# Performance work log

Hardware: AMD Instinct MI355X
Metric: run time of the kernel (lower is better)

The kernel has to match this reference:

```python
import jax, jax.numpy as jnp
import numpy as np

SCALE_DTYPE = jnp.float32

def rotate_half(x):
    half = x.shape[-1] // 2
    return jnp.concatenate([-x[..., half:], x[..., :half]], axis=-1)

def apply_rope(x, cos, sin):
    # x: [B,T,H,Dh]; cos/sin: [T,Dh] -> broadcast to [1,T,1,Dh]
    c = cos[None, :, None, :]
    s = sin[None, :, None, :]
    return x * c + rotate_half(x) * s

def setup_inputs() -> dict:
    key = jax.random.key(0)
    ks = jax.random.split(key, 7)
    B, T, D, H, Dh = 4, 2048, 1024, 16, 64
    x = jax.random.normal(ks[0], (B, T, D), dtype=jnp.float32)
    cos = jax.random.uniform(ks[1], (T, Dh), dtype=jnp.float32)
    sin = jax.random.uniform(ks[2], (T, Dh), dtype=jnp.float32)
    scale = 1.0 / np.sqrt(D)
    Wq = jax.random.normal(ks[3], (D, D), dtype=jnp.float32) * scale
    Wk = jax.random.normal(ks[4], (D, D), dtype=jnp.float32) * scale
    Wv = jax.random.normal(ks[5], (D, D), dtype=jnp.float32) * scale
    Wo = jax.random.normal(ks[6], (D, D), dtype=jnp.float32) * scale
    return {"x": x, "cos": cos, "sin": sin, "Wq": Wq, "Wk": Wk, "Wv": Wv, "Wo": Wo}

def reference(x, cos, sin, Wq, Wk, Wv, Wo):
    B, T, D = x.shape
    H, Dh = 16, 64
    # Linear projections (weights stored [in, out]) and split heads
    q = (x @ Wq).reshape(B, T, H, Dh)
    k = (x @ Wk).reshape(B, T, H, Dh)
    v = (x @ Wv).reshape(B, T, H, Dh)
    q = apply_rope(q, cos[:T], sin[:T])
    k = apply_rope(k, cos[:T], sin[:T])
    scale = 1.0 / jnp.sqrt(jnp.asarray(Dh, dtype=x.dtype))
    # [B,H,T,T] causal scores
    scores = jnp.einsum('bthd,bshd->bhts', q, k) * scale
    causal = jnp.tril(jnp.ones((T, T), dtype=bool))
    scores = jnp.where(causal[None, None, :, :], scores, jnp.asarray(-jnp.inf, dtype=scores.dtype))
    weights = jax.nn.softmax(scores, axis=-1)
    out = jnp.einsum('bhts,bshd->bthd', weights, v).reshape(B, T, D)
    return out @ Wo
```

## Files before the change

### kernel.cpp

```cpp
#include <hip/hip_runtime.h>
#include <cstdint>
#include <cstddef>

typedef unsigned short ushort_t;
typedef __attribute__((ext_vector_type(8))) short short8;
typedef __attribute__((ext_vector_type(4))) float float4v;
typedef __attribute__((ext_vector_type(4))) unsigned short ushort4v;

__device__ __forceinline__ float b2f(ushort_t u) {
    uint32_t x = ((uint32_t)u) << 16;
    float f;
    __builtin_memcpy(&f, &x, 4);
    return f;
}
__device__ __forceinline__ ushort_t f2b(float f) {
    uint32_t x;
    __builtin_memcpy(&x, &f, 4);
    uint32_t r = (x + 0x7fffu + ((x >> 16) & 1u)) >> 16;
    return (ushort_t)r;
}
__device__ __forceinline__ ushort_t f2b_trunc(float f) {
    uint32_t x;
    __builtin_memcpy(&x, &f, 4);
    return (ushort_t)(x >> 16);
}

typedef __attribute__((address_space(3))) void lds_void;
typedef __attribute__((address_space(1))) const void gbl_void;
__device__ __forceinline__ void gload16(const void* g, void* l) {
    __builtin_amdgcn_global_load_lds((gbl_void*)(uintptr_t)g, (lds_void*)(uintptr_t)l, 16, 0, 0);
}

__global__ void detect_dtype(const ushort_t* __restrict__ cosp, int* __restrict__ flag) {
    int tid = threadIdx.x;
    int bad = 0;
    for (int i = tid; i < 512; i += 64) {
        ushort_t u = cosp[i];
        int sign = u >> 15;
        int e = (u >> 7) & 0xFF;
        if (sign || e > 126) bad = 1;
    }
    int anybad = __any(bad);
    if (tid == 0) *flag = anybad ? 1 : 0;
}

__global__ __launch_bounds__(256) void convert_x(const void* __restrict__ in,
                                                 ushort_t* __restrict__ out,
                                                 const int* __restrict__ flag) {
    if (*flag == 0) return;
    int i = (blockIdx.x * 256 + threadIdx.x) * 4;
    float4v v = *(const float4v*)((const float*)in + i);
    ushort4v o;
#pragma unroll
    for (int j = 0; j < 4; ++j) o[j] = f2b(v[j]);
    *(ushort4v*)(out + i) = o;
}

__global__ __launch_bounds__(256) void convert_cs(const void* __restrict__ c,
                                                  const void* __restrict__ s,
                                                  ushort_t* __restrict__ cb,
                                                  ushort_t* __restrict__ sb,
                                                  const int* __restrict__ flag) {
    int f = *flag;
    int i = blockIdx.x * 256 + threadIdx.x;
    if (i >= 131072) return;
    if (f) {
        cb[i] = f2b(((const float*)c)[i]);
        sb[i] = f2b(((const float*)s)[i]);
    } else {
        cb[i] = ((const ushort_t*)c)[i];
        sb[i] = ((const ushort_t*)s)[i];
    }
}

__global__ __launch_bounds__(256) void transpose_w4(const void* __restrict__ w0,
                                                    const void* __restrict__ w1,
                                                    const void* __restrict__ w2,
                                                    const void* __restrict__ w3,
                                                    ushort_t* __restrict__ out,
                                                    const int* __restrict__ flag) {
    int f = *flag;
    int z = blockIdx.z;
    const void* in = (z == 0) ? w0 : (z == 1) ? w1 : (z == 2) ? w2 : w3;
    ushort_t* o = out + (size_t)z * 1024 * 1024;
    __shared__ ushort_t tile[32][33];
    int bx = blockIdx.x * 32;
    int by = blockIdx.y * 32;
    int tx = threadIdx.x & 31;
    int ty = threadIdx.x >> 5;
    for (int r = ty; r < 32; r += 8) {
        size_t idx = (size_t)(by + r) * 1024 + bx + tx;
        tile[r][tx] = f ? f2b(((const float*)in)[idx]) : ((const ushort_t*)in)[idx];
    }
    __syncthreads();
    for (int r = ty; r < 32; r += 8)
        o[(size_t)(bx + r) * 1024 + by + tx] = tile[tx][r];
}

template <int W>
__device__ __forceinline__ void vm_wait() {
    if constexpr (W == 6)      asm volatile("s_waitcnt vmcnt(6)" ::: "memory");
    else                       asm volatile("s_waitcnt vmcnt(0)" ::: "memory");
}
#define KBAR()                                       \
    do {                                             \
        asm volatile("" ::: "memory");               \
        __builtin_amdgcn_s_barrier();                \
        asm volatile("" ::: "memory");               \
    } while (0)

__global__ __launch_bounds__(512, 2) void gemm_qkv(const ushort_t* __restrict__ X0,
                                                   const ushort_t* __restrict__ X1,
                                                   const ushort_t* __restrict__ Wt,
                                                   ushort_t* __restrict__ qk,
                                                   ushort_t* __restrict__ vt,
                                                   const ushort_t* __restrict__ cosb,
                                                   const ushort_t* __restrict__ sinb,
                                                   const int* __restrict__ flagp) {
    __shared__ ushort_t LDS[73728];
    char* LDSc = (char*)LDS;

    int tid = threadIdx.x;
    int lane = tid & 63;
    int wave = tid >> 6;
    int wm = wave >> 1;
    int wn = wave & 1;
    int quad = lane >> 4;
    int l16 = lane & 15;

    int id = blockIdx.x;
    int xcd = id & 7;
    int r = id >> 3;
    int m0 = (xcd * 4 + (r & 3)) * 256;
    int n0 = (r >> 2) * 128;

    const ushort_t* Xb = (*flagp) ? X1 : X0;

    int lrow = lane >> 3;
    int lslot = (lane & 7) ^ lrow;
    const ushort_t* aSrc = Xb + (size_t)(m0 + wave * 32 + lrow) * 1024 + lslot * 8;
    const ushort_t* bSrc = Wt + (size_t)(n0 + wave * 16 + lrow) * 1024 + lslot * 8;
    int ldsA_w = (wave * 32) * 128;
    int ldsB_w = (wave * 16) * 128;

    int aoff0 = (wm * 64 + l16) * 128 + ((quad ^ (l16 & 7)) * 16);
    int aoff1 = (wm * 64 + l16) * 128 + (((4 + quad) ^ (l16 & 7)) * 16);
    int boff0 = (wn * 64 + l16) * 128 + ((quad ^ (l16 & 7)) * 16);
    int boff1 = (wn * 64 + l16) * 128 + (((4 + quad) ^ (l16 & 7)) * 16);

    float4v acc[4][4];
#pragma unroll
    for (int i = 0; i < 4; ++i)
#pragma unroll
        for (int n = 0; n < 4; ++n) acc[i][n] = (float4v){0.f, 0.f, 0.f, 0.f};

#define STAGE6(t, jj)                                                       \
    do {                                                                    \
        const ushort_t* as_ = aSrc + (jj) * 64;                             \
        const ushort_t* bs_ = bSrc + (jj) * 64;                             \
        char* al_ = LDSc + (t) * 32768 + ldsA_w;                            \
        char* bl_ = LDSc + 98304 + (t) * 16384 + ldsB_w;                    \
        gload16(as_, al_);                                                  \
        gload16(as_ + 8 * 1024, al_ + 1024);                                \
        gload16(as_ + 16 * 1024, al_ + 2048);                               \
        gload16(as_ + 24 * 1024, al_ + 3072);                               \
        gload16(bs_, bl_);                                                  \
        gload16(bs_ + 8 * 1024, bl_ + 1024);                                \
    } while (0)

#define COMPUTE(t)                                                          \
    do {                                                                    \
        const char* ab_ = LDSc + (t) * 32768;                               \
        const char* bb_ = LDSc + 98304 + (t) * 16384;                       \
        short8 a0_[4], b0_[4], a1_[4], b1_[4];                              \
        _Pragma("unroll") for (int i = 0; i < 4; ++i) {                     \
            a0_[i] = *(const short8*)(ab_ + aoff0 + i * 2048);              \
            a1_[i] = *(const short8*)(ab_ + aoff1 + i * 2048);              \
        }                                                                   \
        _Pragma("unroll") for (int n = 0; n < 4; ++n) {                     \
            b0_[n] = *(const short8*)(bb_ + boff0 + n * 2048);              \
            b1_[n] = *(const short8*)(bb_ + boff1 + n * 2048);              \
        }                                                                   \
        __builtin_amdgcn_s_setprio(1);                                      \
        _Pragma("unroll") for (int i = 0; i < 4; ++i)                       \
            _Pragma("unroll") for (int n = 0; n < 4; ++n)                   \
                acc[i][n] = __builtin_amdgcn_mfma_f32_16x16x32_bf16(        \
                    a0_[i], b0_[n], acc[i][n], 0, 0, 0);                    \
        _Pragma("unroll") for (int i = 0; i < 4; ++i)                       \
            _Pragma("unroll") for (int n = 0; n < 4; ++n)                   \
                acc[i][n] = __builtin_amdgcn_mfma_f32_16x16x32_bf16(        \
                    a1_[i], b1_[n], acc[i][n], 0, 0, 0);                    \
        __builtin_amdgcn_s_setprio(0);                                      \
    } while (0)

    STAGE6(0, 0);
    STAGE6(1, 1);
    vm_wait<6>();
    KBAR();

#pragma unroll 1
    for (int g = 0; g < 4; ++g) {
        int j = g * 3;
        STAGE6(2, j + 2);
        COMPUTE(0);
        vm_wait<6>();
        KBAR();
        STAGE6(0, j + 3);
        COMPUTE(1);
        vm_wait<6>();
        KBAR();
        STAGE6(1, j + 4);
        COMPUTE(2);
        vm_wait<6>();
        KBAR();
    }
    STAGE6(2, 14);
    COMPUTE(0);
    vm_wait<6>();
    KBAR();
    STAGE6(0, 15);
    COMPUTE(1);
    vm_wait<6>();
    KBAR();
    COMPUTE(2);
    vm_wait<0>();
    KBAR();
    COMPUTE(0);

#undef STAGE6
#undef COMPUTE

    int nglob = n0 + wn * 64;
    int region = nglob >> 10;
    int hcol = (nglob & 1023) >> 6;

    if (region < 2) {
        float scl = (region == 0) ? 0.18033688f : 1.0f;
        int colbase = region * 1024 + hcol * 64 + l16;
#pragma unroll
        for (int i = 0; i < 4; ++i) {
            int rowb = m0 + wm * 64 + i * 16 + quad * 4;
#pragma unroll
            for (int rr = 0; rr < 4; ++rr) {
                int row = rowb + rr;
                int t = row & 2047;
                const ushort_t* cp = cosb + t * 64 + l16;
                const ushort_t* sp = sinb + t * 64 + l16;
                float c0 = b2f(cp[0]), c1 = b2f(cp[16]), c2 = b2f(cp[32]), c3 = b2f(cp[48]);
                float s0v = b2f(sp[0]), s1v = b2f(sp[16]), s2v = b2f(sp[32]), s3v = b2f(sp[48]);
                float a0 = acc[i][0][rr], a1 = acc[i][1][rr], a2 = acc[i][2][rr], a3 = acc[i][3][rr];
                float o0 = (a0 * c0 - a2 * s0v) * scl;
                float o1 = (a1 * c1 - a3 * s1v) * scl;
                float o2 = (a2 * c2 + a0 * s2v) * scl;
                float o3 = (a3 * c3 + a1 * s3v) * scl;
                size_t base = (size_t)row * 2048 + colbase;
                qk[base] = f2b(o0);
                qk[base + 16] = f2b(o1);
                qk[base + 32] = f2b(o2);
                qk[base + 48] = f2b(o3);
            }
        }
    } else {
#pragma unroll
        for (int i = 0; i < 4; ++i) {
            int rowb = m0 + wm * 64 + i * 16 + quad * 4;
            int b = rowb >> 11;
            int t0 = rowb & 2047;
            size_t hb = (size_t)(b * 16 + hcol) * 64;
#pragma unroll
            for (int n = 0; n < 4; ++n) {
                int d = l16 + n * 16;
                ushort4v pk;
#pragma unroll
                for (int rr = 0; rr < 4; ++rr) pk[rr] = f2b(acc[i][n][rr]);
                *(ushort4v*)(vt + (hb + d) * 2048 + t0) = pk;
            }
        }
    }
}

__global__ __launch_bounds__(256) void gemm_proj(const ushort_t* __restrict__ A, int lda,
                                                 const ushort_t* __restrict__ Bt,
                                                 void* __restrict__ C, int ldc,
                                                 int K,
                                                 const int* __restrict__ flagp) {
    __shared__ ushort_t Al[128 * 64];
    __shared__ ushort_t Bl[128 * 64];

    int tid = threadIdx.x;
    int lane = tid & 63;
    int wave = tid >> 6;
    int wr = wave >> 1;
    int wc = wave & 1;
    int quad = lane >> 4;
    int l16 = lane & 15;

    int id = blockIdx.x;
    int xcd = id & 7;
    int t = id >> 3;
    int m0 = (xcd * 8 + (t & 7)) * 128;
    int n0 = (t >> 3) * 128;

    int lrow = lane >> 3;
    int lcol = (lane & 7) * 8;

    float4v acc[4][4];
#pragma unroll
    for (int i = 0; i < 4; ++i)
#pragma unroll
        for (int j = 0; j < 4; ++j) acc[i][j] = (float4v){0.f, 0.f, 0.f, 0.f};

    for (int k0 = 0; k0 < K; k0 += 64) {
        __syncthreads();
#pragma unroll
        for (int p = 0; p < 4; ++p) {
            int row = wave * 32 + p * 8 + lrow;
            gload16(A + (size_t)(m0 + row) * lda + k0 + lcol, &Al[(size_t)(wave * 4 + p) * 512]);
            gload16(Bt + (size_t)(n0 + row) * K + k0 + lcol, &Bl[(size_t)(wave * 4 + p) * 512]);
        }
        __syncthreads();

#pragma unroll
        for (int ks = 0; ks < 2; ++ks) {
            int kf = ks * 32 + quad * 8;
            short8 a_frag[4], b_frag[4];
#pragma unroll
            for (int i = 0; i < 4; ++i) {
                a_frag[i] = *(const short8*)(&Al[(wr * 64 + i * 16 + l16) * 64 + kf]);
                b_frag[i] = *(const short8*)(&Bl[(wc * 64 + i * 16 + l16) * 64 + kf]);
            }
#pragma unroll
            for (int i = 0; i < 4; ++i)
#pragma unroll
                for (int j = 0; j < 4; ++j)
                    acc[i][j] = __builtin_amdgcn_mfma_f32_16x16x32_bf16(
                        a_frag[i], b_frag[j], acc[i][j], 0, 0, 0);
        }
    }

    int f32out = *flagp;

#pragma unroll
    for (int i = 0; i < 4; ++i) {
        int rowb = m0 + wr * 64 + i * 16 + quad * 4;
#pragma unroll
        for (int r = 0; r < 4; ++r) {
            size_t base = (size_t)(rowb + r) * ldc + n0 + wc * 64 + l16;
            if (f32out) {
                float* Cf = (float*)C;
#pragma unroll
                for (int j = 0; j < 4; ++j) Cf[base + j * 16] = acc[i][j][r];
            } else {
                ushort_t* Cb = (ushort_t*)C;
#pragma unroll
                for (int j = 0; j < 4; ++j) Cb[base + j * 16] = f2b(acc[i][j][r]);
            }
        }
    }
}

__global__ __launch_bounds__(512, 4) void attn_mfma(ushort_t* qk,
                                                    const ushort_t* __restrict__ vt) {
    __shared__ ushort_t Kl[2][4096];
    __shared__ ushort_t Vl[2][4096];
    __shared__ ushort_t Pl[8 * 16 * 72];

    int tid = threadIdx.x;
    int lane = tid & 63;
    int wave = tid >> 6;
    int quad = lane >> 4;
    int l16 = lane & 15;

    int id = blockIdx.x;
    int bxi = (id >> 3) & 7;
    int bh = (id & 7) * 8 + (id >> 6);
    int b = bh >> 4;
    int h = bh & 15;

    ushort_t* Pw = &Pl[wave * 16 * 72];

    int rr = tid >> 3;
    int sl = (tid & 7) ^ (rr & 7);
    const ushort_t* ksrc = qk + (size_t)(b * 2048 + rr) * 2048 + 1024 + h * 64 + sl * 8;
    const ushort_t* vsrc = vt + (size_t)(bh * 64 + rr) * 2048 + sl * 8;
    char* kdst = (char*)&Kl[0][0] + wave * 1024;
    char* vdst = (char*)&Vl[0][0] + wave * 1024;

    int swr = l16 & 7;

#pragma unroll 1
    for (int phase = 0; phase < 2; ++phase) {
        int qt = phase ? bxi : (15 - bxi);
        int row0 = qt * 128 + wave * 16;
        size_t qbase = ((size_t)(b * 2048 + row0)) * 2048 + h * 64;

        short8 qf[2];
        {
            const ushort_t* p = qk + qbase + (size_t)l16 * 2048 + quad * 8;
            qf[0] = *(const short8*)p;
            qf[1] = *(const short8*)(p + 32);
        }

        float4v oacc[4];
#pragma unroll
        for (int nt = 0; nt < 4; ++nt) oacc[nt] = (float4v){0.f, 0.f, 0.f, 0.f};
        float psum[4];
#pragma unroll
        for (int r = 0; r < 4; ++r) psum[r] = 0.f;

        int ntiles = 2 * qt + 2;

        gload16(ksrc, kdst);
        gload16(vsrc, vdst);
        vm_wait<0>();
        KBAR();

        for (int st = 0; st < ntiles; ++st) {
            int s0 = st * 64;
            int buf = st & 1;

            if (st + 1 < ntiles) {
                gload16(ksrc + (size_t)(s0 + 64) * 2048, kdst + ((st + 1) & 1) * 8192);
                gload16(vsrc + (s0 + 64), vdst + ((st + 1) & 1) * 8192);
            }

            if (s0 <= row0 + 15) {
                const char* kb = (const char*)&Kl[buf][0];
                const char* vb = (const char*)&Vl[buf][0];

                float4v sacc[4];
#pragma unroll
                for (int ct = 0; ct < 4; ++ct) sacc[ct] = (float4v){0.f, 0.f, 0.f, 0.f};
#pragma unroll
                for (int ks = 0; ks < 2; ++ks) {
                    short8 bfr[4];
#pragma unroll
                    for (int ct = 0; ct < 4; ++ct)
                        bfr[ct] = *(const short8*)(kb + (ct * 16 + l16) * 128 +
                                                   (((ks * 4 + quad) ^ swr) * 16));
                    __builtin_amdgcn_s_setprio(1);
#pragma unroll
                    for (int ct = 0; ct < 4; ++ct)
                        sacc[ct] = __builtin_amdgcn_mfma_f32_16x16x32_bf16(
                            qf[ks], bfr[ct], sacc[ct], 0, 0, 0);
                    __builtin_amdgcn_s_setprio(0);
                }

                if ((s0 + 63) > row0) {
#pragma unroll
                    for (int r = 0; r < 4; ++r) {
                        int trow = row0 + quad * 4 + r;
                        float ps = 0.f;
#pragma unroll
                        for (int ct = 0; ct < 4; ++ct) {
                            float p = exp2f(sacc[ct][r]);
                            if ((s0 + ct * 16 + l16) > trow) p = 0.f;
                            ps += p;
                            Pw[(quad * 4 + r) * 72 + ct * 16 + l16] = f2b_trunc(p);
                        }
                        psum[r] += ps;
                    }
                } else {
#pragma unroll
                    for (int r = 0; r < 4; ++r) {
                        float ps = 0.f;
#pragma unroll
                        for (int ct = 0; ct < 4; ++ct) {
                            float p = exp2f(sacc[ct][r]);
                            ps += p;
                            Pw[(quad * 4 + r) * 72 + ct * 16 + l16] = f2b_trunc(p);
                        }
                        psum[r] += ps;
                    }
                }

#pragma unroll
                for (int ks = 0; ks < 2; ++ks) {
                    short8 bfr[4];
#pragma unroll
                    for (int nt = 0; nt < 4; ++nt)
                        bfr[nt] = *(const short8*)(vb + (nt * 16 + l16) * 128 +
                                                   (((ks * 4 + quad) ^ swr) * 16));
                    short8 af = *(const short8*)(&Pw[l16 * 72 + ks * 32 + quad * 8]);
                    __builtin_amdgcn_s_setprio(1);
#pragma unroll
                    for (int nt = 0; nt < 4; ++nt)
                        oacc[nt] = __builtin_amdgcn_mfma_f32_16x16x32_bf16(
                            af, bfr[nt], oacc[nt], 0, 0, 0);
                    __builtin_amdgcn_s_setprio(0);
                }
            }

            vm_wait<0>();
            KBAR();
        }

#pragma unroll
        for (int r = 0; r < 4; ++r) {
            float ps = psum[r];
#pragma unroll
            for (int off = 1; off < 16; off <<= 1) ps += __shfl_xor(ps, off);
            float inv = 1.0f / ps;
            size_t base = qbase + (size_t)(quad * 4 + r) * 2048;
#pragma unroll
            for (int nt = 0; nt < 4; ++nt)
                qk[base + nt * 16 + l16] = f2b(oacc[nt][r] * inv);
        }
    }
}

extern "C" void kernel_launch(void* const* d_in, const int* in_sizes, int n_in,
                              void* d_out, int out_size, void* d_ws, size_t ws_size,
                              hipStream_t stream) {
    const void* x = d_in[0];
    const void* cosp = d_in[1];
    const void* sinp = d_in[2];
    const void* Wq = d_in[3];
    const void* Wk = d_in[4];
    const void* Wv = d_in[5];
    const void* Wo = d_in[6];

    char* ws = (char*)d_ws;
    int* flag = (int*)ws;
    ushort_t* vtg = (ushort_t*)(ws + 256);
    ushort_t* qk = vtg + (size_t)8192 * 2048;
    ushort_t* WT = qk + (size_t)8192 * 2048;
    ushort_t* WoT = WT + (size_t)3 * 1024 * 1024;
    ushort_t* cosb = WT + (size_t)4 * 1024 * 1024;
    ushort_t* sinb = cosb + (size_t)2048 * 64;
    ushort_t* xb = sinb + (size_t)2048 * 64;

    detect_dtype<<<1, 64, 0, stream>>>((const ushort_t*)cosp, flag);
    convert_cs<<<512, 256, 0, stream>>>(cosp, sinp, cosb, sinb, flag);
    convert_x<<<8192, 256, 0, stream>>>(x, xb, flag);
    transpose_w4<<<dim3(32, 32, 4), 256, 0, stream>>>(Wq, Wk, Wv, Wo, WT, flag);

    gemm_qkv<<<768, 512, 0, stream>>>((const ushort_t*)x, xb, WT, qk, vtg, cosb, sinb, flag);

    attn_mfma<<<512, 512, 0, stream>>>(qk, vtg);

    gemm_proj<<<512, 256, 0, stream>>>(qk, 2048, WoT, d_out, 1024, 1024, flag);
}
```

Measured before the change: 273.3 us.

## Merge prep kernels and triple-buffer output projection GEMM with swizzled LDS

Merges the three preprocessing kernels (cos/sin convert, x convert, weight transpose) into one launch split by blockIdx.z, removing two launch gaps. Rewrites the output-projection GEMM to use 256x128 tiles with 512 threads, a three-stage global-to-LDS pipeline with partial vmcnt waits and one barrier per stage, XOR-swizzled LDS layout to cut bank conflicts, and raised MFMA priority. It uses more LDS per block and launches half as many blocks, which may reduce occupancy and load balance.

New measurement: 241.5 us, median of 2. 11.6% less time.

```diff
diff --git a/kernel.cpp b/kernel.cpp
--- a/kernel.cpp
+++ b/kernel.cpp
@@ -44,57 +44,56 @@
     if (tid == 0) *flag = anybad ? 1 : 0;
 }
 
-__global__ __launch_bounds__(256) void convert_x(const void* __restrict__ in,
-                                                 ushort_t* __restrict__ out,
-                                                 const int* __restrict__ flag) {
-    if (*flag == 0) return;
-    int i = (blockIdx.x * 256 + threadIdx.x) * 4;
-    float4v v = *(const float4v*)((const float*)in + i);
-    ushort4v o;
-#pragma unroll
-    for (int j = 0; j < 4; ++j) o[j] = f2b(v[j]);
-    *(ushort4v*)(out + i) = o;
-}
-
-__global__ __launch_bounds__(256) void convert_cs(const void* __restrict__ c,
-                                                  const void* __restrict__ s,
-                                                  ushort_t* __restrict__ cb,
-                                                  ushort_t* __restrict__ sb,
-                                                  const int* __restrict__ flag) {
+__global__ __launch_bounds__(256) void prep_all(const void* __restrict__ x,
+                                                ushort_t* __restrict__ xb,
+                                                const void* __restrict__ c,
+                                                const void* __restrict__ s,
+                                                ushort_t* __restrict__ cb,
+                                                ushort_t* __restrict__ sb,
+                                                const void* __restrict__ w0,
+                                                const void* __restrict__ w1,
+                                                const void* __restrict__ w2,
+                                                const void* __restrict__ w3,
+                                                ushort_t* __restrict__ wt,
+                                                const int* __restrict__ flag) {
+    __shared__ ushort_t tile[32][33];
+    int z = blockIdx.z;
     int f = *flag;
-    int i = blockIdx.x * 256 + threadIdx.x;
-    if (i >= 131072) return;
-    if (f) {
-        cb[i] = f2b(((const float*)c)[i]);
-        sb[i] = f2b(((const float*)s)[i]);
+    if (z < 4) {
+        const void* in = (z == 0) ? w0 : (z == 1) ? w1 : (z == 2) ? w2 : w3;
+        ushort_t* o = wt + (size_t)z * 1024 * 1024;
+        int bx = blockIdx.x * 32;
+        int by = blockIdx.y * 32;
+        int tx = threadIdx.x & 31;
+        int ty = threadIdx.x >> 5;
+        for (int r = ty; r < 32; r += 8) {
+            size_t idx = (size_t)(by + r) * 1024 + bx + tx;
+            tile[r][tx] = f ? f2b(((const float*)in)[idx]) : ((const ushort_t*)in)[idx];
+        }
+        __syncthreads();
+        for (int r = ty; r < 32; r += 8)
+            o[(size_t)(bx + r) * 1024 + by + tx] = tile[tx][r];
+    } else if (z == 4) {
+        int i = (blockIdx.y * 32 + blockIdx.x) * 256 + threadIdx.x;
+        if (i < 131072) {
+            if (f) {
+                cb[i] = f2b(((const float*)c)[i]);
+                sb[i] = f2b(((const float*)s)[i]);
+            } else {
+                cb[i] = ((const ushort_t*)c)[i];
+                sb[i] = ((const ushort_t*)s)[i];
+            }
+        }
     } else {
-        cb[i] = ((const ushort_t*)c)[i];
-        sb[i] = ((const ushort_t*)s)[i];
-    }
-}
-
-__global__ __launch_bounds__(256) void transpose_w4(const void* __restrict__ w0,
-                                                    const void* __restrict__ w1,
-                                                    const void* __restrict__ w2,
-                                                    const void* __restrict__ w3,
-                                                    ushort_t* __restrict__ out,
-                                                    const int* __restrict__ flag) {
-    int f = *flag;
-    int z = blockIdx.z;
-    const void* in = (z == 0) ? w0 : (z == 1) ? w1 : (z == 2) ? w2 : w3;
-    ushort_t* o = out + (size_t)z * 1024 * 1024;
-    __shared__ ushort_t tile[32][33];
-    int bx = blockIdx.x * 32;
-    int by = blockIdx.y * 32;
-    int tx = threadIdx.x & 31;
-    int ty = threadIdx.x >> 5;
-    for (int r = ty; r < 32; r += 8) {
-        size_t idx = (size_t)(by + r) * 1024 + bx + tx;
-        tile[r][tx] = f ? f2b(((const float*)in)[idx]) : ((const ushort_t*)in)[idx];
-    }
-    __syncthreads();
-    for (int r = ty; r < 32; r += 8)
-        o[(size_t)(bx + r) * 1024 + by + tx] = tile[tx][r];
+        if (f == 0) return;
+        int bid = (z - 5) * 1024 + blockIdx.y * 32 + blockIdx.x;
+        int i = (bid * 256 + threadIdx.x) * 4;
+        float4v v = *(const float4v*)((const float*)x + i);
+        ushort4v o4;
+#pragma unroll
+        for (int j = 0; j < 4; ++j) o4[j] = f2b(v[j]);
+        *(ushort4v*)(xb + i) = o4;
+    }
 }
 
 template <int W>
@@ -279,81 +278,139 @@
     }
 }
 
-__global__ __launch_bounds__(256) void gemm_proj(const ushort_t* __restrict__ A, int lda,
-                                                 const ushort_t* __restrict__ Bt,
-                                                 void* __restrict__ C, int ldc,
-                                                 int K,
-                                                 const int* __restrict__ flagp) {
-    __shared__ ushort_t Al[128 * 64];
-    __shared__ ushort_t Bl[128 * 64];
+__global__ __launch_bounds__(512, 2) void gemm_proj(const ushort_t* __restrict__ A, int lda,
+                                                    const ushort_t* __restrict__ Bt,
+                                                    void* __restrict__ C, int ldc,
+                                                    int K,
+                                                    const int* __restrict__ flagp) {
+    __shared__ ushort_t LDS[73728];
+    char* LDSc = (char*)LDS;
 
     int tid = threadIdx.x;
     int lane = tid & 63;
     int wave = tid >> 6;
-    int wr = wave >> 1;
-    int wc = wave & 1;
+    int wm = wave >> 1;
+    int wn = wave & 1;
     int quad = lane >> 4;
     int l16 = lane & 15;
 
     int id = blockIdx.x;
     int xcd = id & 7;
-    int t = id >> 3;
-    int m0 = (xcd * 8 + (t & 7)) * 128;
-    int n0 = (t >> 3) * 128;
+    int r = id >> 3;
+    int m0 = (xcd * 4 + (r & 3)) * 256;
+    int n0 = (r >> 2) * 128;
 
     int lrow = lane >> 3;
-    int lcol = (lane & 7) * 8;
+    int lslot = (lane & 7) ^ lrow;
+    const ushort_t* aSrc = A + (size_t)(m0 + wave * 32 + lrow) * lda + lslot * 8;
+    const ushort_t* bSrc = Bt + (size_t)(n0 + wave * 16 + lrow) * K + lslot * 8;
+    int ldsA_w = (wave * 32) * 128;
+    int ldsB_w = (wave * 16) * 128;
+    int astr = 8 * lda;
+    int bstr = 8 * K;
+
+    int aoff0 = (wm * 64 + l16) * 128 + ((quad ^ (l16 & 7)) * 16);
+    int aoff1 = (wm * 64 + l16) * 128 + (((4 + quad) ^ (l16 & 7)) * 16);
+    int boff0 = (wn * 64 + l16) * 128 + ((quad ^ (l16 & 7)) * 16);
+    int boff1 = (wn * 64 + l16) * 128 + (((4 + quad) ^ (l16 & 7)) * 16);
 
     float4v acc[4][4];
 #pragma unroll
     for (int i = 0; i < 4; ++i)
 #pragma unroll
-        for (int j = 0; j < 4; ++j) acc[i][j] = (float4v){0.f, 0.f, 0.f, 0.f};
-
-    for (int k0 = 0; k0 < K; k0 += 64) {
-        __syncthreads();
-#pragma unroll
-        for (int p = 0; p < 4; ++p) {
-            int row = wave * 32 + p * 8 + lrow;
-            gload16(A + (size_t)(m0 + row) * lda + k0 + lcol, &Al[(size_t)(wave * 4 + p) * 512]);
-            gload16(Bt + (size_t)(n0 + row) * K + k0 + lcol, &Bl[(size_t)(wave * 4 + p) * 512]);
-        }
-        __syncthreads();
-
-#pragma unroll
-        for (int ks = 0; ks < 2; ++ks) {
-            int kf = ks * 32 + quad * 8;
-            short8 a_frag[4], b_frag[4];
-#pragma unroll
-            for (int i = 0; i < 4; ++i) {
-                a_frag[i] = *(const short8*)(&Al[(wr * 64 + i * 16 + l16) * 64 + kf]);
-                b_frag[i] = *(const short8*)(&Bl[(wc * 64 + i * 16 + l16) * 64 + kf]);
-            }
-#pragma unroll
-            for (int i = 0; i < 4; ++i)
-#pragma unroll
-                for (int j = 0; j < 4; ++j)
-                    acc[i][j] = __builtin_amdgcn_mfma_f32_16x16x32_bf16(
-                        a_frag[i], b_frag[j], acc[i][j], 0, 0, 0);
-        }
-    }
+        for (int n = 0; n < 4; ++n) acc[i][n] = (float4v){0.f, 0.f, 0.f, 0.f};
+
+#define STAGE6P(t, jj)                                                      \
+    do {                                                                    \
+        const ushort_t* as_ = aSrc + (jj) * 64;                             \
+        const ushort_t* bs_ = bSrc + (jj) * 64;                             \
+        char* al_ = LDSc + (t) * 32768 + ldsA_w;                            \
+        char* bl_ = LDSc + 98304 + (t) * 16384 + ldsB_w;                    \
+        gload16(as_, al_);                                                  \
+        gload16(as_ + astr, al_ + 1024);                                    \
+        gload16(as_ + 2 * astr, al_ + 2048);                                \
+        gload16(as_ + 3 * astr, al_ + 3072);                                \
+        gload16(bs_, bl_);                                                  \
+        gload16(bs_ + bstr, bl_ + 1024);                                    \
+    } while (0)
+
+#define COMPUTEP(t)                                                         \
+    do {                                                                    \
+        const char* ab_ = LDSc + (t) * 32768;                               \
+        const char* bb_ = LDSc + 98304 + (t) * 16384;                       \
+        short8 a0_[4], b0_[4], a1_[4], b1_[4];                              \
+        _Pragma("unroll") for (int i = 0; i < 4; ++i) {                     \
+            a0_[i] = *(const short8*)(ab_ + aoff0 + i * 2048);              \
+            a1_[i] = *(const short8*)(ab_ + aoff1 + i * 2048);              \
+        }                                                                   \
+        _Pragma("unroll") for (int n = 0; n < 4; ++n) {                     \
+            b0_[n] = *(const short8*)(bb_ + boff0 + n * 2048);              \
+            b1_[n] = *(const short8*)(bb_ + boff1 + n * 2048);              \
+        }                                                                   \
+        __builtin_amdgcn_s_setprio(1);                                      \
+        _Pragma("unroll") for (int i = 0; i < 4; ++i)                       \
+            _Pragma("unroll") for (int n = 0; n < 4; ++n)                   \
+                acc[i][n] = __builtin_amdgcn_mfma_f32_16x16x32_bf16(        \
+                    a0_[i], b0_[n], acc[i][n], 0, 0, 0);                    \
+        _Pragma("unroll") for (int i = 0; i < 4; ++i)                       \
+            _Pragma("unroll") for (int n = 0; n < 4; ++n)                   \
+                acc[i][n] = __builtin_amdgcn_mfma_f32_16x16x32_bf16(        \
+                    a1_[i], b1_[n], acc[i][n], 0, 0, 0);                    \
+        __builtin_amdgcn_s_setprio(0);                                      \
+    } while (0)
+
+    STAGE6P(0, 0);
+    STAGE6P(1, 1);
+    vm_wait<6>();
+    KBAR();
+
+#pragma unroll 1
+    for (int g = 0; g < 4; ++g) {
+        int j = g * 3;
+        STAGE6P(2, j + 2);
+        COMPUTEP(0);
+        vm_wait<6>();
+        KBAR();
+        STAGE6P(0, j + 3);
+        COMPUTEP(1);
+        vm_wait<6>();
+        KBAR();
+        STAGE6P(1, j + 4);
+        COMPUTEP(2);
+        vm_wait<6>();
+        KBAR();
+    }
+    STAGE6P(2, 14);
+    COMPUTEP(0);
+    vm_wait<6>();
+    KBAR();
+    STAGE6P(0, 15);
+    COMPUTEP(1);
+    vm_wait<6>();
+    KBAR();
+    COMPUTEP(2);
+    vm_wait<0>();
+    KBAR();
+    COMPUTEP(0);
+
+#undef STAGE6P
+#undef COMPUTEP
 
     int f32out = *flagp;
-
 #pragma unroll
     for (int i = 0; i < 4; ++i) {
-        int rowb = m0 + wr * 64 + i * 16 + quad * 4;
-#pragma unroll
-        for (int r = 0; r < 4; ++r) {
-            size_t base = (size_t)(rowb + r) * ldc + n0 + wc * 64 + l16;
+        int rowb = m0 + wm * 64 + i * 16 + quad * 4;
+#pragma unroll
+        for (int rr = 0; rr < 4; ++rr) {
+            size_t base = (size_t)(rowb + rr) * ldc + n0 + wn * 64 + l16;
             if (f32out) {
                 float* Cf = (float*)C;
 #pragma unroll
-                for (int j = 0; j < 4; ++j) Cf[base + j * 16] = acc[i][j][r];
+                for (int n = 0; n < 4; ++n) Cf[base + n * 16] = acc[i][n][rr];
             } else {
                 ushort_t* Cb = (ushort_t*)C;
 #pragma unroll
-                for (int j = 0; j < 4; ++j) Cb[base + j * 16] = f2b(acc[i][j][r]);
+                for (int n = 0; n < 4; ++n) Cb[base + n * 16] = f2b(acc[i][n][rr]);
             }
         }
     }
@@ -531,13 +588,12 @@
     ushort_t* xb = sinb + (size_t)2048 * 64;
 
     detect_dtype<<<1, 64, 0, stream>>>((const ushort_t*)cosp, flag);
-    convert_cs<<<512, 256, 0, stream>>>(cosp, sinp, cosb, sinb, flag);
-    convert_x<<<8192, 256, 0, stream>>>(x, xb, flag);
-    transpose_w4<<<dim3(32, 32, 4), 256, 0, stream>>>(Wq, Wk, Wv, Wo, WT, flag);
+    prep_all<<<dim3(32, 32, 13), 256, 0, stream>>>(x, xb, cosp, sinp, cosb, sinb,
+                                                   Wq, Wk, Wv, Wo, WT, flag);
 
     gemm_qkv<<<768, 512, 0, stream>>>((const ushort_t*)x, xb, WT, qk, vtg, cosb, sinb, flag);
 
     attn_mfma<<<512, 512, 0, stream>>>(qk, vtg);
 
-    gemm_proj<<<512, 256, 0, stream>>>(qk, 2048, WoT, d_out, 1024, 1024, flag);
-}
+    gemm_proj<<<256, 512, 0, stream>>>(qk, 2048, WoT, d_out, 1024, 1024, flag);
+}
```
